# Kernel optimization log

Hardware: AMD Instinct MI355X
Metric: run time of the kernel (lower is better)

Reference implementation:

```python
import math
import jax, jax.numpy as jnp
import numpy as np

W_BITS = 8
A_BITS = 8
N_HEADS = 16

def fake_quant(x, bits):
    # symmetric per-tensor fake quantization with straight-through estimator
    if bits >= 32:
        return x
    qmax = float(2 ** (bits - 1) - 1)
    scale = jnp.maximum(jnp.max(jnp.abs(x)) / qmax, 1e-8)
    q = jnp.round(x / scale) * scale
    return x + jax.lax.stop_gradient(q - x)

def qlinear(x, W, b):
    # QuantizeLinear: quantize activations (a_bits) and weights (w_bits), then y = x @ W^T + b
    xq = fake_quant(x, A_BITS)
    Wq = fake_quant(W, W_BITS)
    return jnp.einsum('bsd,ed->bse', xq, Wq) + b

def setup_inputs() -> dict:
    key = jax.random.key(0)
    B, S, D = 2, 2048, 1024
    ks = jax.random.split(key, 6)
    inp = {
        'hidden_states': jax.random.normal(ks[0], (B, S, D), dtype=jnp.float32),
        'attention_mask': jnp.ones((B, S), dtype=jnp.float32),
        'Wq': 0.02 * jax.random.normal(ks[1], (D, D), dtype=jnp.float32),
        'bq': jnp.zeros((D,), dtype=jnp.float32),
        'Wk': 0.02 * jax.random.normal(ks[2], (D, D), dtype=jnp.float32),
        'bk': jnp.zeros((D,), dtype=jnp.float32),
        'Wv': 0.02 * jax.random.normal(ks[3], (D, D), dtype=jnp.float32),
        'bv': jnp.zeros((D,), dtype=jnp.float32),
        'Wo': 0.02 * jax.random.normal(ks[4], (D, D), dtype=jnp.float32),
        'bo': jnp.zeros((D,), dtype=jnp.float32),
    }
    return inp

def reference(hidden_states, attention_mask, Wq, bq, Wk, bk, Wv, bv, Wo, bo):
    B, S, D = hidden_states.shape
    H = N_HEADS
    hd = D // H

    q = qlinear(hidden_states, Wq, bq).reshape(B, S, H, hd)
    k = qlinear(hidden_states, Wk, bk).reshape(B, S, H, hd)
    v = qlinear(hidden_states, Wv, bv).reshape(B, S, H, hd)

    # scores: [B, H, Sq, Sk]
    scores = jnp.einsum('bqhd,bkhd->bhqk', q, k) / math.sqrt(hd)
    mask_bias = (1.0 - attention_mask)[:, None, None, :] * -10000.0
    scores = scores + mask_bias
    probs = jax.nn.softmax(scores, axis=-1)

    attn = jnp.einsum('bhqk,bkhd->bqhd', probs, v).reshape(B, S, D)
    return qlinear(attn, Wo, bo)
```

## Files before the change

### kernel.cpp

```cpp
#include <hip/hip_runtime.h>
#include <cstddef>
#include <cstdint>

constexpr int Bb = 2, Ss = 2048, Dd = 1024, Hh = 16, HD = 64;
constexpr int Mm = Bb * Ss;

typedef int v4i __attribute__((ext_vector_type(4)));
typedef __bf16 bf16x8 __attribute__((ext_vector_type(8)));
typedef __bf16 bf16x2 __attribute__((ext_vector_type(2)));
typedef float f32x16 __attribute__((ext_vector_type(16)));

#define QPOSTMUL 0.18033688f

__device__ __forceinline__ float qscale(float amax) {
    return fmaxf(amax / 127.0f, 1e-8f);
}

__device__ __forceinline__ unsigned short bf16rtn(float x) {
    __bf16 b = (__bf16)x;
    return __builtin_bit_cast(unsigned short, b);
}

__device__ __forceinline__ unsigned pack_bf16x2(float a, float b) {
    bf16x2 h;
    h[0] = (__bf16)a;
    h[1] = (__bf16)b;
    return __builtin_bit_cast(unsigned, h);
}

__global__ void amax_all(const float4* __restrict__ hidden,
                         const float4* __restrict__ w0, const float4* __restrict__ w1,
                         const float4* __restrict__ w2, const float4* __restrict__ w3,
                         unsigned* __restrict__ slots) {
    const float4* src; int n4, slot, bx, nb;
    if (blockIdx.x < 448) { src = hidden; n4 = Mm * Dd / 4; slot = 0; bx = blockIdx.x; nb = 448; }
    else {
        int w = (blockIdx.x - 448) >> 4; bx = (blockIdx.x - 448) & 15; nb = 16;
        src = w == 0 ? w0 : w == 1 ? w1 : w == 2 ? w2 : w3;
        n4 = Dd * Dd / 4; slot = 1 + w;
    }
    float m = 0.f;
    for (int i = bx * blockDim.x + threadIdx.x; i < n4; i += nb * blockDim.x) {
        float4 v = src[i];
        m = fmaxf(m, fmaxf(fmaxf(fabsf(v.x), fabsf(v.y)), fmaxf(fabsf(v.z), fabsf(v.w))));
    }
    #pragma unroll
    for (int off = 32; off > 0; off >>= 1) m = fmaxf(m, __shfl_down(m, off, 64));
    __shared__ float sm[4];
    int lane = threadIdx.x & 63, wid = threadIdx.x >> 6;
    if (lane == 0) sm[wid] = m;
    __syncthreads();
    if (threadIdx.x == 0) {
        float mm = fmaxf(fmaxf(sm[0], sm[1]), fmaxf(sm[2], sm[3]));
        atomicMax(slots + slot, __float_as_uint(mm));
    }
}

__global__ void quant_all(const float* __restrict__ hidden,
                          const float* __restrict__ w0, const float* __restrict__ w1,
                          const float* __restrict__ w2, const float* __restrict__ w3,
                          const float* __restrict__ amax,
                          char* __restrict__ hq8, char* __restrict__ Wall8) {
    const float* x; char* y; int n4, slot, bx, nb;
    if (blockIdx.x < 1024) { x = hidden; y = hq8; n4 = Mm * Dd / 4; slot = 0; bx = blockIdx.x; nb = 1024; }
    else {
        int w = (blockIdx.x - 1024) >> 5; bx = (blockIdx.x - 1024) & 31; nb = 32;
        x = w == 0 ? w0 : w == 1 ? w1 : w == 2 ? w2 : w3;
        y = Wall8 + ((size_t)w << 20);
        n4 = Dd * Dd / 4; slot = 1 + w;
    }
    float s = qscale(amax[slot]);
    const float4* x4 = (const float4*)x;
    char4* y4 = (char4*)y;
    for (int i = bx * blockDim.x + threadIdx.x; i < n4; i += nb * blockDim.x) {
        float4 v = x4[i];
        char4 q;
        q.x = (char)(int)rintf(v.x / s);
        q.y = (char)(int)rintf(v.y / s);
        q.z = (char)(int)rintf(v.z / s);
        q.w = (char)(int)rintf(v.w / s);
        y4[i] = q;
    }
}

__global__ void quant_a(const float* __restrict__ x, char* __restrict__ y,
                        const float* __restrict__ amax, int n4) {
    float s = qscale(amax[0]);
    int stride = gridDim.x * blockDim.x;
    const float4* x4 = (const float4*)x;
    char4* y4 = (char4*)y;
    for (int i = blockIdx.x * blockDim.x + threadIdx.x; i < n4; i += stride) {
        float4 v = x4[i];
        char4 q;
        q.x = (char)(int)rintf(v.x / s);
        q.y = (char)(int)rintf(v.y / s);
        q.z = (char)(int)rintf(v.z / s);
        q.w = (char)(int)rintf(v.w / s);
        y4[i] = q;
    }
}

#define GLOAD_LDS16(g, l) __builtin_amdgcn_global_load_lds( \
    (const __attribute__((address_space(1))) unsigned int*)(g), \
    (__attribute__((address_space(3))) unsigned int*)(l), 16, 0, 0)

__device__ __forceinline__ void gemm128_core(const char* __restrict__ A, const char* __restrict__ Bw,
                                             int bm, int bn, int K, int t,
                                             char* At, char* Bt, v4i acc[4][4]) {
    const int lane = t & 63, w = t >> 6;
    const int wm = (w >> 1) * 64, wn = (w & 1) * 64;
    const int lr = lane & 15, kq = lane >> 4;
    const int rs = w * 16 + (lane >> 2);
    const int cc = lane & 3;
    const int NT = K / 64;

    auto stage = [&](int s, int buf) {
        int k0 = s * 64;
        char* Ab = At + buf * 16384;
        char* Bb = Bt + buf * 16384;
        #pragma unroll
        for (int h = 0; h < 2; h++) {
            int r = rs + h * 64;
            int cs = cc ^ ((r >> 1) & 3);
            GLOAD_LDS16(A  + (size_t)(bm + r) * K + k0 + cs * 16, Ab + r * 64 + cc * 16);
            GLOAD_LDS16(Bw + (size_t)(bn + r) * K + k0 + cs * 16, Bb + r * 64 + cc * 16);
        }
    };

    stage(0, 0);
    __syncthreads();
    for (int s = 0; s < NT; s++) {
        const int cur = s & 1;
        if (s + 1 < NT) stage(s + 1, cur ^ 1);

        const char* Ac = At + cur * 16384;
        const char* Bc = Bt + cur * 16384;
        v4i af[4], bf[4];
        #pragma unroll
        for (int mt = 0; mt < 4; mt++) {
            int row = wm + mt * 16 + lr;
            af[mt] = *(const v4i*)(Ac + row * 64 + ((kq ^ ((row >> 1) & 3)) << 4));
        }
        #pragma unroll
        for (int nt = 0; nt < 4; nt++) {
            int row = wn + nt * 16 + lr;
            bf[nt] = *(const v4i*)(Bc + row * 64 + ((kq ^ ((row >> 1) & 3)) << 4));
        }
        #pragma unroll
        for (int mt = 0; mt < 4; mt++)
            #pragma unroll
            for (int nt = 0; nt < 4; nt++)
                acc[mt][nt] = __builtin_amdgcn_mfma_i32_16x16x64_i8(af[mt], bf[nt], acc[mt][nt], 0, 0, 0);

        if (s + 1 < NT) __syncthreads();
    }
}

__global__ __launch_bounds__(256) void gemm_qkv(const char* __restrict__ A,
                                                const char* __restrict__ Wall8,
                                                const float* __restrict__ bq,
                                                const float* __restrict__ bk,
                                                const float* __restrict__ bv,
                                                const float* __restrict__ amax,
                                                unsigned short* __restrict__ qb16,
                                                unsigned short* __restrict__ kb16,
                                                unsigned short* __restrict__ vt16) {
    __shared__ alignas(16) char pool[34816];
    char* At = pool;
    char* Bt = pool + 8192;
    unsigned short (*Tt)[136] = (unsigned short(*)[136])pool;

    const int t = threadIdx.x, lane = t & 63, w = t >> 6;
    const int mat = blockIdx.x >> 3;
    const int bn = (blockIdx.x & 7) * 128, bm = blockIdx.y * 128;
    const int wm = (w >> 1) * 64, wn = (w & 1) * 64;
    const int lr = lane & 15, kq = lane >> 4;

    const v4i vzero = {0, 0, 0, 0};
    v4i acc[4][4];
    #pragma unroll
    for (int mt = 0; mt < 4; mt++)
        #pragma unroll
        for (int nt = 0; nt < 4; nt++) acc[mt][nt] = vzero;

    const char* Bw = Wall8 + ((size_t)mat << 20);
    gemm128_core(A, Bw, bm, bn, Dd, t, At, Bt, acc);

    const float* bias = mat == 0 ? bq : mat == 1 ? bk : bv;
    float sc = qscale(amax[0]) * qscale(amax[1 + mat]);
    float pm = (mat == 0) ? QPOSTMUL : 1.0f;

    __syncthreads();

    if (mat != 2) {
        #pragma unroll
        for (int nt = 0; nt < 4; nt++) {
            int n_l = wn + nt * 16 + lr;
            float bv_ = bias[bn + n_l];
            #pragma unroll
            for (int mt = 0; mt < 4; mt++) {
                int m_l = wm + mt * 16 + kq * 4;
                #pragma unroll
                for (int rg = 0; rg < 4; rg++)
                    Tt[m_l + rg][n_l] = bf16rtn(((float)acc[mt][nt][rg] * sc + bv_) * pm);
            }
        }
    } else {
        #pragma unroll
        for (int nt = 0; nt < 4; nt++) {
            int n_l = wn + nt * 16 + lr;
            float bv_ = bias[bn + n_l];
            #pragma unroll
            for (int mt = 0; mt < 4; mt++) {
                int m_l = wm + mt * 16 + kq * 4;
                ushort4 hv;
                hv.x = bf16rtn((float)acc[mt][nt][0] * sc + bv_);
                hv.y = bf16rtn((float)acc[mt][nt][1] * sc + bv_);
                hv.z = bf16rtn((float)acc[mt][nt][2] * sc + bv_);
                hv.w = bf16rtn((float)acc[mt][nt][3] * sc + bv_);
                *(ushort4*)&Tt[n_l][m_l] = hv;
            }
        }
    }
    __syncthreads();

    {
        int row = t >> 1, half = t & 1;
        unsigned short* dst;
        if (mat != 2) {
            dst = (mat == 0 ? qb16 : kb16) + (size_t)(bm + row) * Dd + bn + half * 64;
        } else {
            int n = bn + row;
            int e = n & 63, hc = n >> 6;
            int b_ = bm >> 11, s_ = (bm & 2047) + half * 64;
            dst = vt16 + (((size_t)(b_ * Hh + hc) * 64 + e) * Ss) + s_;
        }
        const unsigned short* srcl = &Tt[row][half * 64];
        #pragma unroll
        for (int c = 0; c < 8; c++)
            *(int4*)(dst + c * 8) = *(const int4*)(srcl + c * 8);
    }
}

__global__ __launch_bounds__(256) void gemm_o(const char* __restrict__ A,
                                              const char* __restrict__ Bw,
                                              const float* __restrict__ bias,
                                              const float* __restrict__ amaxA,
                                              const float* __restrict__ amaxB,
                                              float* __restrict__ C) {
    __shared__ alignas(16) char pool[24576];
    const int t = threadIdx.x, lane = t & 63, w = t >> 6;
    const int bn = blockIdx.x * 64, bm = blockIdx.y * 128;
    const int wm = (w >> 1) * 64, wn = (w & 1) * 32;
    const int lr = lane & 15, kq = lane >> 4;
    const int rs = t >> 2, cc = t & 3;
    const int cs = cc ^ ((rs >> 1) & 3);
    const int rs2 = rs + 64, cs2 = cc ^ ((rs2 >> 1) & 3);

    auto stage = [&](int s, int buf) {
        int k0 = s * 64;
        char* Ab = pool + buf * 12288;
        char* Bb = Ab + 8192;
        GLOAD_LDS16(A  + (size_t)(bm + rs)  * Dd + k0 + cs  * 16, Ab + rs  * 64 + cc * 16);
        GLOAD_LDS16(A  + (size_t)(bm + rs2) * Dd + k0 + cs2 * 16, Ab + rs2 * 64 + cc * 16);
        GLOAD_LDS16(Bw + (size_t)(bn + rs)  * Dd + k0 + cs  * 16, Bb + rs  * 64 + cc * 16);
    };

    const v4i vzero = {0, 0, 0, 0};
    v4i acc[4][2];
    #pragma unroll
    for (int mt = 0; mt < 4; mt++) { acc[mt][0] = vzero; acc[mt][1] = vzero; }

    stage(0, 0);
    __syncthreads();
    const int NT = Dd / 64;
    for (int s = 0; s < NT; s++) {
        const int cur = s & 1;
        if (s + 1 < NT) stage(s + 1, cur ^ 1);

        const char* Ac = pool + cur * 12288;
        const char* Bc = Ac + 8192;
        v4i af[4], bf[2];
        #pragma unroll
        for (int mt = 0; mt < 4; mt++) {
            int row = wm + mt * 16 + lr;
            af[mt] = *(const v4i*)(Ac + row * 64 + ((kq ^ ((row >> 1) & 3)) << 4));
        }
        #pragma unroll
        for (int nt = 0; nt < 2; nt++) {
            int row = wn + nt * 16 + lr;
            bf[nt] = *(const v4i*)(Bc + row * 64 + ((kq ^ ((row >> 1) & 3)) << 4));
        }
        #pragma unroll
        for (int mt = 0; mt < 4; mt++)
            #pragma unroll
            for (int nt = 0; nt < 2; nt++)
                acc[mt][nt] = __builtin_amdgcn_mfma_i32_16x16x64_i8(af[mt], bf[nt], acc[mt][nt], 0, 0, 0);

        if (s + 1 < NT) __syncthreads();
    }

    float sc = qscale(amaxA[0]) * qscale(amaxB[0]);
    #pragma unroll
    for (int nt = 0; nt < 2; nt++) {
        int n = bn + wn + nt * 16 + lr;
        float bv_ = bias[n];
        #pragma unroll
        for (int mt = 0; mt < 4; mt++)
            #pragma unroll
            for (int rg = 0; rg < 4; rg++) {
                int m = bm + wm + mt * 16 + kq * 4 + rg;
                C[(size_t)m * Dd + n] = (float)acc[mt][nt][rg] * sc + bv_;
            }
    }
}

__global__ __launch_bounds__(512, 4) void attn_mfma(
    const unsigned short* __restrict__ qb16, const unsigned short* __restrict__ kb16,
    const unsigned short* __restrict__ vt16,
    const float* __restrict__ mask, float* __restrict__ Ob, unsigned* __restrict__ amax_out) {
    __shared__ alignas(16) char apool[36864];
    unsigned short (*Ks)[64][72] = (unsigned short(*)[64][72])apool;
    unsigned short (*Vs)[64][72] = (unsigned short(*)[64][72])(apool + 18432);
    __shared__ float wred[4];

    const int t = threadIdx.x, lane = t & 63, wq = t >> 6;
    const int g = wq >> 2, wq4 = wq & 3, tg = t & 255;
    const int ln31 = lane & 31, h5 = lane >> 5;
    const int b = blockIdx.z, h = blockIdx.y, q0 = blockIdx.x * 128;
    const int kbase = g << 10;

    bf16x8 qf[4];
    {
        int qrow = q0 + wq4 * 32 + ln31;
        const unsigned short* qb_ = qb16 + ((size_t)(b * Ss + qrow)) * Dd + h * 64 + h5 * 8;
        #pragma unroll
        for (int c = 0; c < 4; c++) qf[c] = *(const bf16x8*)(qb_ + c * 16);
    }

    const int srow = tg >> 2, cp = (tg & 3) * 2;
    const int rho = (srow >> 1) + (srow & 1) * 32;
    int4 pk0, pk1, pv0, pv1; float pmv = 1.f;
    auto prefetch = [&](int k0) {
        const unsigned short* gk = kb16 + ((size_t)(b * Ss + k0 + srow)) * Dd + h * 64 + cp * 8;
        const unsigned short* gv = vt16 + (((size_t)(b * Hh + h) * 64 + srow)) * Ss + k0 + cp * 8;
        pk0 = *(const int4*)gk; pk1 = *(const int4*)(gk + 8);
        pv0 = *(const int4*)gv; pv1 = *(const int4*)(gv + 8);
        pmv = mask[b * Ss + k0 + lane];
    };

    f32x16 o0 = 0.f, o1 = 0.f;
    float la0 = 0.f, la1 = 0.f, la2 = 0.f, la3 = 0.f;

    prefetch(kbase);
    for (int k0 = kbase; k0 < kbase + Ss / 2; k0 += 64) {
        __syncthreads();
        *(int4*)&Ks[g][rho][cp * 8]      = pk0;
        *(int4*)&Ks[g][rho][cp * 8 + 8]  = pk1;
        *(int4*)&Vs[g][srow][cp * 8]     = pv0;
        *(int4*)&Vs[g][srow][cp * 8 + 8] = pv1;
        unsigned long long bm = __ballot(pmv > 0.5f);
        __syncthreads();
        if (k0 + 64 < kbase + Ss / 2) prefetch(k0 + 64);

        f32x16 sc0 = 0.f, sc1 = 0.f;
        __builtin_amdgcn_s_setprio(1);
        #pragma unroll
        for (int c = 0; c < 4; c++) {
            bf16x8 kh0 = *(const bf16x8*)&Ks[g][ln31][c * 16 + h5 * 8];
            bf16x8 kh1 = *(const bf16x8*)&Ks[g][32 + ln31][c * 16 + h5 * 8];
            sc0 = __builtin_amdgcn_mfma_f32_32x32x16_bf16(kh0, qf[c], sc0, 0, 0, 0);
            sc1 = __builtin_amdgcn_mfma_f32_32x32x16_bf16(kh1, qf[c], sc1, 0, 0, 0);
        }
        __builtin_amdgcn_s_setprio(0);

        #pragma unroll
        for (int c = 0; c < 4; c++) {
            float e0[4], e1[4];
            #pragma unroll
            for (int j = 0; j < 4; j++) {
                e0[j] = __builtin_amdgcn_exp2f(sc0[4 * c + j]);
                e1[j] = __builtin_amdgcn_exp2f(sc1[4 * c + j]);
            }
            if (bm != ~0ull) {
                #pragma unroll
                for (int j = 0; j < 4; j++) {
                    int kk = 16 * c + 8 * h5 + 2 * j;
                    e0[j] *= (float)(int)((bm >> kk) & 1);
                    e1[j] *= (float)(int)((bm >> (kk + 1)) & 1);
                }
            }
            la0 += e0[0] + e1[0];
            la1 += e0[1] + e1[1];
            la2 += e0[2] + e1[2];
            la3 += e0[3] + e1[3];

            uint4 pw;
            pw.x = pack_bf16x2(e0[0], e1[0]);
            pw.y = pack_bf16x2(e0[1], e1[1]);
            pw.z = pack_bf16x2(e0[2], e1[2]);
            pw.w = pack_bf16x2(e0[3], e1[3]);
            bf16x8 pf = __builtin_bit_cast(bf16x8, pw);
            bf16x8 vh0 = *(const bf16x8*)&Vs[g][ln31][c * 16 + h5 * 8];
            bf16x8 vh1 = *(const bf16x8*)&Vs[g][32 + ln31][c * 16 + h5 * 8];
            __builtin_amdgcn_s_setprio(1);
            o0 = __builtin_amdgcn_mfma_f32_32x32x16_bf16(pf, vh0, o0, 0, 0, 0);
            o1 = __builtin_amdgcn_mfma_f32_32x32x16_bf16(pf, vh1, o1, 0, 0, 0);
            __builtin_amdgcn_s_setprio(0);
        }
    }

    float lsum = (la0 + la1) + (la2 + la3);
    lsum += __shfl_xor(lsum, 32, 64);

    __syncthreads();
    float (*Osh)[65] = (float(*)[65])apool;
    float (*Lsh2)[128] = (float(*)[128])(apool + 33280);

    if (lane < 32) Lsh2[g][wq4 * 32 + ln31] = lsum;
    if (g == 1) {
        #pragma unroll
        for (int r = 0; r < 16; r++) {
            int rl = wq4 * 32 + (r & 3) + 8 * (r >> 2) + 4 * h5;
            Osh[rl][ln31]      = o0[r];
            Osh[rl][32 + ln31] = o1[r];
        }
    }
    __syncthreads();
    if (g == 0) {
        float lmax = 0.f;
        #pragma unroll
        for (int r = 0; r < 16; r++) {
            int rl = wq4 * 32 + (r & 3) + 8 * (r >> 2) + 4 * h5;
            float inv = 1.0f / (Lsh2[0][rl] + Lsh2[1][rl]);
            size_t ro = ((size_t)(b * Ss + q0 + rl)) * Dd + h * 64;
            float v0 = (o0[r] + Osh[rl][ln31]) * inv;
            float v1 = (o1[r] + Osh[rl][32 + ln31]) * inv;
            Ob[ro + ln31]      = v0;
            Ob[ro + 32 + ln31] = v1;
            lmax = fmaxf(lmax, fmaxf(fabsf(v0), fabsf(v1)));
        }
        #pragma unroll
        for (int off = 32; off > 0; off >>= 1) lmax = fmaxf(lmax, __shfl_xor(lmax, off, 64));
        if (lane == 0) wred[wq4] = lmax;
    }
    __syncthreads();
    if (t == 0) {
        float m = fmaxf(fmaxf(wred[0], wred[1]), fmaxf(wred[2], wred[3]));
        atomicMax(amax_out, __float_as_uint(m));
    }
}

extern "C" void kernel_launch(void* const* d_in, const int* in_sizes, int n_in,
                              void* d_out, int out_size, void* d_ws, size_t ws_size,
                              hipStream_t stream) {
    const float* hidden = (const float*)d_in[0];
    const float* mask   = (const float*)d_in[1];
    const float* Wq = (const float*)d_in[2];
    const float* bq = (const float*)d_in[3];
    const float* Wk = (const float*)d_in[4];
    const float* bk = (const float*)d_in[5];
    const float* Wv = (const float*)d_in[6];
    const float* bv = (const float*)d_in[7];
    const float* Wo = (const float*)d_in[8];
    const float* bo = (const float*)d_in[9];
    float* out = (float*)d_out;

    char* ws = (char*)d_ws;
    float* scal = (float*)ws;
    size_t off = 1024;
    const size_t szH8 = (size_t)Mm * Dd;
    const size_t szHb = (size_t)Mm * Dd * sizeof(unsigned short);
    const size_t szHf = (size_t)Mm * Dd * sizeof(float);
    char* hq8   = ws + off; off += szH8;
    char* Wall8 = ws + off; off += 4u << 20;
    char* aq8   = ws + off; off += szH8;
    unsigned short* qb16 = (unsigned short*)(ws + off); off += szHb;
    unsigned short* kb16 = (unsigned short*)(ws + off); off += szHb;
    unsigned short* vt16 = (unsigned short*)(ws + off); off += szHb;
    float* ab = (float*)(ws + off); off += szHf;

    hipMemsetAsync(scal, 0, 64, stream);

    amax_all<<<512, 256, 0, stream>>>((const float4*)hidden, (const float4*)Wq,
                                      (const float4*)Wk, (const float4*)Wv, (const float4*)Wo,
                                      (unsigned*)scal);
    quant_all<<<1152, 256, 0, stream>>>(hidden, Wq, Wk, Wv, Wo, scal, hq8, Wall8);

    gemm_qkv<<<dim3(24, 32), 256, 0, stream>>>(hq8, Wall8, bq, bk, bv, scal,
                                               qb16, kb16, vt16);

    attn_mfma<<<dim3(Ss / 128, Hh, Bb), 512, 0, stream>>>(qb16, kb16, vt16,
                                                          mask, ab, (unsigned*)(scal + 5));

    quant_a<<<1024, 256, 0, stream>>>(ab, aq8, scal + 5, Mm * Dd / 4);

    gemm_o<<<dim3(16, 32), 256, 0, stream>>>(aq8, Wall8 + (3u << 20), bo,
                                             scal + 5, scal + 4, out);
}
```

Measured before the change: 215.1 us.

## Store attention output as bf16 and remap attention blocks across XCDs

The attention kernel now writes its output in bf16 instead of fp32, and quant_a reads bf16 and processes eight elements per thread. This halves the traffic for the intermediate activation tensor between attention and the output projection quantization. The attention block index is also remapped so that the blocks of each (batch, head) pair land on the same XCD, which should improve L2 reuse of K/V. Rounding to bf16 before the per-tensor int8 quantization can change which integer some values round to, a small accuracy risk.

```diff
diff --git a/kernel.cpp b/kernel.cpp
--- a/kernel.cpp
+++ b/kernel.cpp
@@ -83,20 +83,22 @@
     }
 }
 
-__global__ void quant_a(const float* __restrict__ x, char* __restrict__ y,
-                        const float* __restrict__ amax, int n4) {
+__global__ void quant_a(const unsigned short* __restrict__ x, char* __restrict__ y,
+                        const float* __restrict__ amax, int n8) {
     float s = qscale(amax[0]);
     int stride = gridDim.x * blockDim.x;
-    const float4* x4 = (const float4*)x;
-    char4* y4 = (char4*)y;
-    for (int i = blockIdx.x * blockDim.x + threadIdx.x; i < n4; i += stride) {
-        float4 v = x4[i];
-        char4 q;
-        q.x = (char)(int)rintf(v.x / s);
-        q.y = (char)(int)rintf(v.y / s);
-        q.z = (char)(int)rintf(v.z / s);
-        q.w = (char)(int)rintf(v.w / s);
-        y4[i] = q;
+    const int4* x8 = (const int4*)x;
+    int2* y8 = (int2*)y;
+    for (int i = blockIdx.x * blockDim.x + threadIdx.x; i < n8; i += stride) {
+        int4 v = x8[i];
+        const unsigned short* u = (const unsigned short*)&v;
+        char q[8];
+        #pragma unroll
+        for (int j = 0; j < 8; j++) {
+            float f = (float)__builtin_bit_cast(__bf16, u[j]);
+            q[j] = (char)(int)rintf(f / s);
+        }
+        y8[i] = *(const int2*)q;
     }
 }
 
@@ -318,7 +320,8 @@
 __global__ __launch_bounds__(512, 4) void attn_mfma(
     const unsigned short* __restrict__ qb16, const unsigned short* __restrict__ kb16,
     const unsigned short* __restrict__ vt16,
-    const float* __restrict__ mask, float* __restrict__ Ob, unsigned* __restrict__ amax_out) {
+    const float* __restrict__ mask, unsigned short* __restrict__ Ob,
+    unsigned* __restrict__ amax_out) {
     __shared__ alignas(16) char apool[36864];
     unsigned short (*Ks)[64][72] = (unsigned short(*)[64][72])apool;
     unsigned short (*Vs)[64][72] = (unsigned short(*)[64][72])(apool + 18432);
@@ -327,7 +330,13 @@
     const int t = threadIdx.x, lane = t & 63, wq = t >> 6;
     const int g = wq >> 2, wq4 = wq & 3, tg = t & 255;
     const int ln31 = lane & 31, h5 = lane >> 5;
-    const int b = blockIdx.z, h = blockIdx.y, q0 = blockIdx.x * 128;
+
+    const int L = blockIdx.x + (blockIdx.y << 4) + (blockIdx.z << 8);
+    const int xcd = L & 7, rest = L >> 3;
+    const int qi = rest & 15, gq = rest >> 4;
+    const int gbh = gq * 8 + xcd;
+    const int h = gbh & 15, b = gbh >> 4;
+    const int q0 = qi * 128;
     const int kbase = g << 10;
 
     bf16x8 qf[4];
@@ -434,11 +443,11 @@
             int rl = wq4 * 32 + (r & 3) + 8 * (r >> 2) + 4 * h5;
             float inv = 1.0f / (Lsh2[0][rl] + Lsh2[1][rl]);
             size_t ro = ((size_t)(b * Ss + q0 + rl)) * Dd + h * 64;
-            float v0 = (o0[r] + Osh[rl][ln31]) * inv;
-            float v1 = (o1[r] + Osh[rl][32 + ln31]) * inv;
-            Ob[ro + ln31]      = v0;
-            Ob[ro + 32 + ln31] = v1;
-            lmax = fmaxf(lmax, fmaxf(fabsf(v0), fabsf(v1)));
+            __bf16 b0 = (__bf16)((o0[r] + Osh[rl][ln31]) * inv);
+            __bf16 b1 = (__bf16)((o1[r] + Osh[rl][32 + ln31]) * inv);
+            Ob[ro + ln31]      = __builtin_bit_cast(unsigned short, b0);
+            Ob[ro + 32 + ln31] = __builtin_bit_cast(unsigned short, b1);
+            lmax = fmaxf(lmax, fmaxf(fabsf((float)b0), fabsf((float)b1)));
         }
         #pragma unroll
         for (int off = 32; off > 0; off >>= 1) lmax = fmaxf(lmax, __shfl_xor(lmax, off, 64));
@@ -471,14 +480,13 @@
     size_t off = 1024;
     const size_t szH8 = (size_t)Mm * Dd;
     const size_t szHb = (size_t)Mm * Dd * sizeof(unsigned short);
-    const size_t szHf = (size_t)Mm * Dd * sizeof(float);
     char* hq8   = ws + off; off += szH8;
     char* Wall8 = ws + off; off += 4u << 20;
     char* aq8   = ws + off; off += szH8;
     unsigned short* qb16 = (unsigned short*)(ws + off); off += szHb;
     unsigned short* kb16 = (unsigned short*)(ws + off); off += szHb;
     unsigned short* vt16 = (unsigned short*)(ws + off); off += szHb;
-    float* ab = (float*)(ws + off); off += szHf;
+    unsigned short* ab   = (unsigned short*)(ws + off); off += szHb;
 
     hipMemsetAsync(scal, 0, 64, stream);
 
@@ -493,7 +501,7 @@
     attn_mfma<<<dim3(Ss / 128, Hh, Bb), 512, 0, stream>>>(qb16, kb16, vt16,
                                                           mask, ab, (unsigned*)(scal + 5));
 
-    quant_a<<<1024, 256, 0, stream>>>(ab, aq8, scal + 5, Mm * Dd / 4);
+    quant_a<<<1024, 256, 0, stream>>>(ab, aq8, scal + 5, Mm * Dd / 8);
 
     gemm_o<<<dim3(16, 32), 256, 0, stream>>>(aq8, Wall8 + (3u << 20), bo,
                                              scal + 5, scal + 4, out);
```

After: 213.9 us, median of 3. About the same (-0.5%).
